# Optimization experiments

Hardware: AMD Instinct MI355X
Metric: run time of the kernel (lower is better)

Reference implementation:

```python
import jax, jax.numpy as jnp
import numpy as np

NUM_CLASSES = 33  # labels 0..32; class 0 = background, 32 instances
EPS = 1e-06


def _lovasz_hinge_flat(logits, labels):
    # logits, labels: flat 1-D float arrays (labels in {0,1})
    signs = 2.0 * labels - 1.0
    errors = 1.0 - logits * signs
    order = jnp.argsort(-errors)            # descending sort
    errors_sorted = errors[order]
    gt_sorted = labels[order]
    gts = jnp.sum(gt_sorted)
    intersection = gts - jnp.cumsum(gt_sorted)
    union = gts + jnp.cumsum(1.0 - gt_sorted)
    jaccard = 1.0 - intersection / union
    grad = jnp.concatenate([jaccard[:1], jaccard[1:] - jaccard[:-1]])
    return jnp.dot(jax.nn.relu(errors_sorted), grad)


def _per_sample_loss(y_emb, y_sig, gt_patch):
    # y_emb: [2,H,W] float, y_sig: [1,H,W] float, gt_patch: [1,H,W] int
    # to_onehot(gt)[0, 1:] -> [N,H,W], N = NUM_CLASSES-1 instance channels
    gt_one_hot = jax.nn.one_hot(gt_patch[0], NUM_CLASSES, axis=0, dtype=y_emb.dtype)[1:]
    counts = jnp.sum(gt_one_hot, axis=(1, 2), keepdims=True)          # [N,1,1]
    # per-instance embedding centers: [2,N,1,1]
    centers = jnp.sum(gt_one_hot[None] * y_emb[:, None], axis=(2, 3), keepdims=True) / counts
    instance_sigmas = gt_one_hot[None] * y_sig[:, None]               # [1,N,H,W]
    sigmas = jnp.sum(instance_sigmas, axis=(2, 3), keepdims=True) / counts  # [1,N,1,1]
    var_sigmas = jnp.sum(((instance_sigmas - jax.lax.stop_gradient(sigmas)) * gt_one_hot) ** 2) / counts  # [N,1,1]
    center_dist = jnp.linalg.norm(centers - y_emb[:, None], axis=0)   # [N,H,W]
    probs = jnp.exp(-0.5 * (center_dist / sigmas) ** 2)               # [1,N,H,W]
    logits = (probs * 2.0 - 1.0).reshape(-1)
    labels = jnp.broadcast_to(gt_one_hot[None], probs.shape).reshape(-1)
    return _lovasz_hinge_flat(logits, labels) + jnp.mean(var_sigmas)


def setup_inputs() -> dict:
    key = jax.random.key(0)
    k1, k2, k3 = jax.random.split(key, 3)
    B, H, W = 4, 512, 512
    y_embeddings = jax.random.normal(k1, (B, 2, H, W), dtype=jnp.float32)
    y_sigma = jax.random.uniform(k2, (B, 1, H, W), dtype=jnp.float32)
    y_true = jax.random.randint(k3, (B, 1, H, W), 0, NUM_CLASSES, dtype=jnp.int64)
    return {"y_embeddings": y_embeddings, "y_sigma": y_sigma, "y_true": y_true}


def reference(y_embeddings, y_sigma, y_true):
    # Assumes every sample contains foreground (random labels over 512x512
    # guarantee this w.h.p.), so the torch `if torch.any(gt>0)` branch is taken
    # for all samples and the final loss is the mean over the batch.
    losses = jax.vmap(_per_sample_loss)(y_embeddings, y_sigma, y_true)
    return jnp.mean(losses)
```

## Files before the change

### kernel.cpp

```cpp
#include <hip/hip_runtime.h>

#define HW    262144
#define BNUM  4
#define NC    33
#define NI    32

#define NB     2048
#define BSCALE 128.0f
#define EG     4096
#define ESCALE 2048.0f

typedef unsigned long long ull;

#define W_PART 16384
#define W_FIN  (W_PART + 5 * 33 * 256)

__global__ void __launch_bounds__(256) stats_kernel(
    const float* __restrict__ emb, const float* __restrict__ sig,
    const int* __restrict__ gt, float* __restrict__ ws) {
  int s = blockIdx.y;
  int j = blockIdx.x;
  int t = threadIdx.x;
  int w = t >> 6;
  __shared__ float acc[4][165];
  int bid = s * 64 + j;
  unsigned* wsu = (unsigned*)ws;
  if (t < 64) wsu[bid * 64 + t] = 0u;
  if (bid == 0 && t < 16) wsu[W_FIN + t] = 0u;
  for (int k = t; k < 4 * 165; k += 256) ((float*)acc)[k] = 0.f;
  __syncthreads();
  const float* e0p = emb + (size_t)s * 2 * HW;
  const float* e1p = e0p + HW;
  const float* sp  = sig + (size_t)s * HW;
  const int*   gp  = gt  + (size_t)s * HW;
  #pragma unroll
  for (int i = 0; i < 4; ++i) {
    int idx = j * 4096 + i * 1024 + t * 4;
    int4   lb = *(const int4*)(gp + idx);
    float4 x  = *(const float4*)(e0p + idx);
    float4 y  = *(const float4*)(e1p + idx);
    float4 sg = *(const float4*)(sp + idx);
#define ACC(L, X, Y, SG)                                                   \
    if (L > 0) {                                                           \
      atomicAdd(&acc[w][L], X);        atomicAdd(&acc[w][33 + L], Y);      \
      atomicAdd(&acc[w][66 + L], SG);  atomicAdd(&acc[w][99 + L], (SG)*(SG)); \
      atomicAdd(&acc[w][132 + L], 1.0f);                                   \
    }
    ACC(lb.x, x.x, y.x, sg.x)
    ACC(lb.y, x.y, y.y, sg.y)
    ACC(lb.z, x.z, y.z, sg.z)
    ACC(lb.w, x.w, y.w, sg.w)
#undef ACC
  }
  __syncthreads();
  if (t < 165) {
    float v = acc[0][t] + acc[1][t] + acc[2][t] + acc[3][t];
    ws[W_PART + t * 256 + s * 64 + j] = v;
  }
}

__global__ void __launch_bounds__(512) hist_scan_kernel(
    const float* __restrict__ emb, const int* __restrict__ gt,
    float* __restrict__ ws, float* __restrict__ out) {
  int s  = blockIdx.y;
  int lb = blockIdx.x;
  __shared__ unsigned hist[NB * 4];
  __shared__ float sums[165];
  __shared__ float4 cons[NC];
  __shared__ ull wsum[8];
  __shared__ float red[8];
  __shared__ float vart_s;
  __shared__ int flag;
  int t = threadIdx.x;
  int lane = t & 63, wid = t >> 6;
  for (int k = t; k < NB * 4; k += 512) hist[k] = 0u;
  if (t < 165) {
    const float4* pp = (const float4*)(ws + W_PART + t * 256 + s * 64);
    float sum = 0.f;
    #pragma unroll
    for (int i = 0; i < 16; ++i) { float4 v = pp[i]; sum += v.x + v.y + v.z + v.w; }
    sums[t] = sum;
  }
  __syncthreads();
  if (t >= 1 && t < NC) {
    float c = sums[132 + t];
    float4 C;
    if (c > 0.f) {
      float inv = 1.0f / c;
      float c0 = sums[t] * inv, c1 = sums[33 + t] * inv, sgm = sums[66 + t] * inv;
      float Q = 0.5f / (sgm * sgm) * BSCALE;
      C.x = Q; C.y = -2.0f * Q * c0; C.z = -2.0f * Q * c1;
      C.w = Q * (c0 * c0 + c1 * c1);
    } else {
      C.x = 0.f; C.y = 0.f; C.z = 0.f; C.w = (float)NB;
    }
    cons[t] = C;
  }
  __syncthreads();
  const float* e0p = emb + (size_t)s * 2 * HW;
  const float* e1p = e0p + HW;
  const int*   gp  = gt  + (size_t)s * HW;
  int idx = lb * 2048 + t * 4;
  int4   lbl = *(const int4*)(gp + idx);
  float4 px  = *(const float4*)(e0p + idx);
  float4 py  = *(const float4*)(e1p + idx);
  float4 ss;
  ss.x = fmaf(px.x, px.x, py.x * py.x);
  ss.y = fmaf(px.y, px.y, py.y * py.y);
  ss.z = fmaf(px.z, px.z, py.z * py.z);
  ss.w = fmaf(px.w, px.w, py.w * py.w);
  unsigned* hr = hist + (t & 3);
  #pragma unroll 4
  for (int n = 1; n <= NI; ++n) {
    float4 C = cons[n];
#define ITEM(P0, P1, SV, L)                                            \
    {                                                                  \
      float bf = fmaf(C.x, SV, fmaf(C.y, P0, fmaf(C.z, P1, C.w)));     \
      int ib = (int)bf;                                                \
      bool pos = (L == n);                                             \
      if (pos) ib = min(ib, NB - 1);                                   \
      if (ib < NB) atomicAdd(&hr[ib << 2], pos ? 0x10000u : 1u);       \
    }
    ITEM(px.x, py.x, ss.x, lbl.x)
    ITEM(px.y, py.y, ss.y, lbl.y)
    ITEM(px.z, py.z, ss.z, lbl.z)
    ITEM(px.w, py.w, ss.w, lbl.w)
#undef ITEM
  }
  __syncthreads();
  ull* th = ((ull*)ws) + (size_t)s * NB;
  for (int k = t; k < NB; k += 512) {
    unsigned v = hist[k*4] + hist[k*4+1] + hist[k*4+2] + hist[k*4+3];
    if (v) {
      ull add = ((ull)(v >> 16) << 32) | (v & 0xFFFFu);
      atomicAdd(&th[k], add);
    }
  }
  __syncthreads();
  if (t == 0) {
    __threadfence();
    unsigned* cnt = (unsigned*)(ws + W_FIN);
    flag = (atomicAdd(&cnt[8 + s], 1u) == 127u);
  }
  __syncthreads();
  if (!flag) return;

  unsigned* ep = hist;
  unsigned* en = hist + EG;
  for (int k = t; k < 2 * EG; k += 512) hist[k] = 0u;
  if (wid == 0) {
    float S = 0.f, rcp = 0.f;
    if (lane >= 1 && lane < NC) {
      float c = sums[132 + lane];
      if (c > 0.f) {
        float sg = sums[66 + lane] / c;
        S = sums[99 + lane] - c * sg * sg;
        rcp = 1.0f / c;
      }
    }
    for (int o = 32; o; o >>= 1) {
      S   += __shfl_down(S, o);
      rcp += __shfl_down(rcp, o);
    }
    if (lane == 0) vart_s = S * rcp / (float)NI;
  }
  __syncthreads();
  for (int b = t; b < NB; b += 512) {
    ull v = atomicAdd(&th[b], 0ull);
    unsigned pos = (unsigned)(v >> 32), neg = (unsigned)(v & 0xFFFFFFFFu);
    if (pos | neg) {
      float tc = ((float)b + 0.5f) * (1.0f / BSCALE);
      float ex = __expf(-tc);
      if (pos) {
        float e = 2.0f - 2.0f * ex;
        int k = (int)(e * ESCALE); if (k > EG - 1) k = EG - 1;
        atomicAdd(&ep[k], pos);
      }
      if (neg) {
        float e = 2.0f * ex;
        int k = (int)(e * ESCALE); if (k > EG - 1) k = EG - 1;
        atomicAdd(&en[k], neg);
      }
    }
  }
  __syncthreads();
  const int CH = EG / 512;
  int j0 = t * CH;
  unsigned np = 0, nn = 0;
  for (int k = 0; k < CH; ++k) {
    int b = EG - 1 - (j0 + k);
    np += ep[b]; nn += en[b];
  }
  ull v = ((ull)np << 32) | (ull)nn;
  ull inc = v;
  for (int o = 1; o < 64; o <<= 1) {
    ull u = __shfl_up(inc, o);
    if (lane >= o) inc += u;
  }
  if (lane == 63) wsum[wid] = inc;
  __syncthreads();
  ull offset = 0, total = 0;
  for (int i = 0; i < 8; ++i) {
    ull xr = wsum[i];
    if (i < wid) offset += xr;
    total += xr;
  }
  ull excl = offset + inc - v;
  float P = (float)(unsigned)(total >> 32);
  unsigned p = (unsigned)(excl >> 32), f = (unsigned)(excl & 0xFFFFFFFFu);
  float jprev = 1.0f - (P - (float)p) / (P + (float)f);
  float contrib = 0.f;
  for (int k = 0; k < CH; ++k) {
    int b = EG - 1 - (j0 + k);
    unsigned ap_ = ep[b], an_ = en[b];
    if (ap_ | an_) {
      p += ap_; f += an_;
      float j = 1.0f - (P - (float)p) / (P + (float)f);
      float e = ((float)b + 0.5f) * (2.0f / EG);
      contrib += e * (j - jprev);
      jprev = j;
    }
  }
  for (int o = 32; o; o >>= 1) contrib += __shfl_down(contrib, o);
  if (lane == 0) red[wid] = contrib;
  __syncthreads();
  if (t == 0) {
    float tot = 0.f;
    for (int i = 0; i < 8; ++i) tot += red[i];
    float loss = tot + vart_s;
    float* fin = ws + W_FIN;
    unsigned* cnt = (unsigned*)(fin + 4);
    atomicExch(&fin[s], loss);
    unsigned old = atomicAdd(&cnt[0], 1u);
    if (old == BNUM - 1) {
      float a = 0.f;
      for (int i = 0; i < BNUM; ++i) a += atomicAdd(&fin[i], 0.0f);
      out[0] = a * (1.0f / BNUM);
    }
  }
}

extern "C" void kernel_launch(void* const* d_in, const int* in_sizes, int n_in,
                              void* d_out, int out_size, void* d_ws, size_t ws_size,
                              hipStream_t stream) {
  const float* emb = (const float*)d_in[0];
  const float* sig = (const float*)d_in[1];
  const int*   gt  = (const int*)d_in[2];
  float* out = (float*)d_out;
  float* ws  = (float*)d_ws;

  dim3 gA(64, BNUM);
  stats_kernel<<<gA, 256, 0, stream>>>(emb, sig, gt, ws);
  dim3 gB(128, BNUM);
  hist_scan_kernel<<<gB, 512, 0, stream>>>(emb, gt, ws, out);
}
```

Measured before the change: 120.6 us.

## Fuse stats and histogram kernels with a per-sample grid barrier

Merges the stats kernel and the histogram/scan kernel into one launch of 512 blocks. Each block reads its pixels once, keeps them in registers, and writes partial stats. A spin-wait barrier across the 128 blocks of each sample then lets those partials be summed before binning. Workspace zeroing moves to a hipMemsetAsync, and shared memory for accumulators and histograms is overlaid in a union. This removes the second global read of embeddings and labels, but it depends on all 512 blocks being co-resident to avoid deadlock and adds spin-wait and memset overhead.

```diff
diff --git a/kernel.cpp b/kernel.cpp
--- a/kernel.cpp
+++ b/kernel.cpp
@@ -12,73 +12,85 @@
 
 typedef unsigned long long ull;
 
-#define W_PART 16384
-#define W_FIN  (W_PART + 5 * 33 * 256)
-
-__global__ void __launch_bounds__(256) stats_kernel(
+#define W_CNTA 16384
+#define W_CNTB 16388
+#define W_CNTF 16392
+#define W_FINL 16396
+#define MEMSET_BYTES (16400 * 4)
+#define W_PART 16400
+#define PJ 168
+#define PS (128 * PJ)
+
+union SMem {
+  float acc[8][165];
+  unsigned hist[NB * 4];
+};
+
+__global__ void __launch_bounds__(512, 4) fused_kernel(
     const float* __restrict__ emb, const float* __restrict__ sig,
-    const int* __restrict__ gt, float* __restrict__ ws) {
-  int s = blockIdx.y;
-  int j = blockIdx.x;
-  int t = threadIdx.x;
-  int w = t >> 6;
-  __shared__ float acc[4][165];
-  int bid = s * 64 + j;
-  unsigned* wsu = (unsigned*)ws;
-  if (t < 64) wsu[bid * 64 + t] = 0u;
-  if (bid == 0 && t < 16) wsu[W_FIN + t] = 0u;
-  for (int k = t; k < 4 * 165; k += 256) ((float*)acc)[k] = 0.f;
-  __syncthreads();
-  const float* e0p = emb + (size_t)s * 2 * HW;
-  const float* e1p = e0p + HW;
-  const float* sp  = sig + (size_t)s * HW;
-  const int*   gp  = gt  + (size_t)s * HW;
-  #pragma unroll
-  for (int i = 0; i < 4; ++i) {
-    int idx = j * 4096 + i * 1024 + t * 4;
-    int4   lb = *(const int4*)(gp + idx);
-    float4 x  = *(const float4*)(e0p + idx);
-    float4 y  = *(const float4*)(e1p + idx);
-    float4 sg = *(const float4*)(sp + idx);
-#define ACC(L, X, Y, SG)                                                   \
-    if (L > 0) {                                                           \
-      atomicAdd(&acc[w][L], X);        atomicAdd(&acc[w][33 + L], Y);      \
-      atomicAdd(&acc[w][66 + L], SG);  atomicAdd(&acc[w][99 + L], (SG)*(SG)); \
-      atomicAdd(&acc[w][132 + L], 1.0f);                                   \
-    }
-    ACC(lb.x, x.x, y.x, sg.x)
-    ACC(lb.y, x.y, y.y, sg.y)
-    ACC(lb.z, x.z, y.z, sg.z)
-    ACC(lb.w, x.w, y.w, sg.w)
-#undef ACC
-  }
-  __syncthreads();
-  if (t < 165) {
-    float v = acc[0][t] + acc[1][t] + acc[2][t] + acc[3][t];
-    ws[W_PART + t * 256 + s * 64 + j] = v;
-  }
-}
-
-__global__ void __launch_bounds__(512) hist_scan_kernel(
-    const float* __restrict__ emb, const int* __restrict__ gt,
-    float* __restrict__ ws, float* __restrict__ out) {
-  int s  = blockIdx.y;
-  int lb = blockIdx.x;
-  __shared__ unsigned hist[NB * 4];
+    const int* __restrict__ gt, float* __restrict__ ws,
+    float* __restrict__ out) {
+  __shared__ SMem sm;
   __shared__ float sums[165];
   __shared__ float4 cons[NC];
   __shared__ ull wsum[8];
   __shared__ float red[8];
   __shared__ float vart_s;
   __shared__ int flag;
+
   int t = threadIdx.x;
-  int lane = t & 63, wid = t >> 6;
-  for (int k = t; k < NB * 4; k += 512) hist[k] = 0u;
+  int bid = blockIdx.x;
+  int s = bid >> 7;
+  int lb = bid & 127;
+  int w = t >> 6;
+  int lane = t & 63, wid = w;
+
+  for (int k = t; k < 8 * 165; k += 512) ((float*)sm.acc)[k] = 0.f;
+  __syncthreads();
+  const float* e0p = emb + (size_t)s * 2 * HW;
+  const float* e1p = e0p + HW;
+  const float* sp  = sig + (size_t)s * HW;
+  const int*   gp  = gt  + (size_t)s * HW;
+  int idx = lb * 2048 + t * 4;
+  int4   lbl = *(const int4*)(gp + idx);
+  float4 x   = *(const float4*)(e0p + idx);
+  float4 y   = *(const float4*)(e1p + idx);
+  float4 sg4 = *(const float4*)(sp + idx);
+#define ACC(L, X, Y, SG)                                                     \
+  if (L > 0) {                                                               \
+    atomicAdd(&sm.acc[w][L], X);        atomicAdd(&sm.acc[w][33 + L], Y);    \
+    atomicAdd(&sm.acc[w][66 + L], SG);  atomicAdd(&sm.acc[w][99 + L], (SG)*(SG)); \
+    atomicAdd(&sm.acc[w][132 + L], 1.0f);                                    \
+  }
+  ACC(lbl.x, x.x, y.x, sg4.x)
+  ACC(lbl.y, x.y, y.y, sg4.y)
+  ACC(lbl.z, x.z, y.z, sg4.z)
+  ACC(lbl.w, x.w, y.w, sg4.w)
+#undef ACC
+  __syncthreads();
   if (t < 165) {
-    const float4* pp = (const float4*)(ws + W_PART + t * 256 + s * 64);
+    float v = 0.f;
+    #pragma unroll
+    for (int i = 0; i < 8; ++i) v += sm.acc[i][t];
+    ws[W_PART + s * PS + lb * PJ + t] = v;
+  }
+  {
+    unsigned* cntA = (unsigned*)ws + W_CNTA + s;
+    if (t == 0) {
+      __threadfence();
+      atomicAdd(cntA, 1u);
+      while (atomicAdd(cntA, 0u) < 128u) __builtin_amdgcn_s_sleep(2);
+      __threadfence();
+    }
+    __syncthreads();
+  }
+
+  for (int k = t; k < NB * 4; k += 512) sm.hist[k] = 0u;
+  if (t < 165) {
+    const float* pp = ws + W_PART + s * PS + t;
     float sum = 0.f;
-    #pragma unroll
-    for (int i = 0; i < 16; ++i) { float4 v = pp[i]; sum += v.x + v.y + v.z + v.w; }
+    #pragma unroll 8
+    for (int j = 0; j < 128; ++j) sum += pp[j * PJ];
     sums[t] = sum;
   }
   __syncthreads();
@@ -97,19 +109,12 @@
     cons[t] = C;
   }
   __syncthreads();
-  const float* e0p = emb + (size_t)s * 2 * HW;
-  const float* e1p = e0p + HW;
-  const int*   gp  = gt  + (size_t)s * HW;
-  int idx = lb * 2048 + t * 4;
-  int4   lbl = *(const int4*)(gp + idx);
-  float4 px  = *(const float4*)(e0p + idx);
-  float4 py  = *(const float4*)(e1p + idx);
   float4 ss;
-  ss.x = fmaf(px.x, px.x, py.x * py.x);
-  ss.y = fmaf(px.y, px.y, py.y * py.y);
-  ss.z = fmaf(px.z, px.z, py.z * py.z);
-  ss.w = fmaf(px.w, px.w, py.w * py.w);
-  unsigned* hr = hist + (t & 3);
+  ss.x = fmaf(x.x, x.x, y.x * y.x);
+  ss.y = fmaf(x.y, x.y, y.y * y.y);
+  ss.z = fmaf(x.z, x.z, y.z * y.z);
+  ss.w = fmaf(x.w, x.w, y.w * y.w);
+  unsigned* hr = sm.hist + (t & 3);
   #pragma unroll 4
   for (int n = 1; n <= NI; ++n) {
     float4 C = cons[n];
@@ -121,16 +126,16 @@
       if (pos) ib = min(ib, NB - 1);                                   \
       if (ib < NB) atomicAdd(&hr[ib << 2], pos ? 0x10000u : 1u);       \
     }
-    ITEM(px.x, py.x, ss.x, lbl.x)
-    ITEM(px.y, py.y, ss.y, lbl.y)
-    ITEM(px.z, py.z, ss.z, lbl.z)
-    ITEM(px.w, py.w, ss.w, lbl.w)
+    ITEM(x.x, y.x, ss.x, lbl.x)
+    ITEM(x.y, y.y, ss.y, lbl.y)
+    ITEM(x.z, y.z, ss.z, lbl.z)
+    ITEM(x.w, y.w, ss.w, lbl.w)
 #undef ITEM
   }
   __syncthreads();
   ull* th = ((ull*)ws) + (size_t)s * NB;
   for (int k = t; k < NB; k += 512) {
-    unsigned v = hist[k*4] + hist[k*4+1] + hist[k*4+2] + hist[k*4+3];
+    unsigned v = sm.hist[k*4] + sm.hist[k*4+1] + sm.hist[k*4+2] + sm.hist[k*4+3];
     if (v) {
       ull add = ((ull)(v >> 16) << 32) | (v & 0xFFFFu);
       atomicAdd(&th[k], add);
@@ -139,22 +144,21 @@
   __syncthreads();
   if (t == 0) {
     __threadfence();
-    unsigned* cnt = (unsigned*)(ws + W_FIN);
-    flag = (atomicAdd(&cnt[8 + s], 1u) == 127u);
+    flag = (atomicAdd((unsigned*)ws + W_CNTB + s, 1u) == 127u);
   }
   __syncthreads();
   if (!flag) return;
 
-  unsigned* ep = hist;
-  unsigned* en = hist + EG;
-  for (int k = t; k < 2 * EG; k += 512) hist[k] = 0u;
+  unsigned* ep = sm.hist;
+  unsigned* en = sm.hist + EG;
+  for (int k = t; k < 2 * EG; k += 512) sm.hist[k] = 0u;
   if (wid == 0) {
     float S = 0.f, rcp = 0.f;
     if (lane >= 1 && lane < NC) {
       float c = sums[132 + lane];
       if (c > 0.f) {
-        float sg = sums[66 + lane] / c;
-        S = sums[99 + lane] - c * sg * sg;
+        float sgm = sums[66 + lane] / c;
+        S = sums[99 + lane] - c * sgm * sgm;
         rcp = 1.0f / c;
       }
     }
@@ -228,11 +232,12 @@
     float tot = 0.f;
     for (int i = 0; i < 8; ++i) tot += red[i];
     float loss = tot + vart_s;
-    float* fin = ws + W_FIN;
-    unsigned* cnt = (unsigned*)(fin + 4);
+    float* fin = ws + W_FINL;
     atomicExch(&fin[s], loss);
-    unsigned old = atomicAdd(&cnt[0], 1u);
+    __threadfence();
+    unsigned old = atomicAdd((unsigned*)ws + W_CNTF, 1u);
     if (old == BNUM - 1) {
+      __threadfence();
       float a = 0.f;
       for (int i = 0; i < BNUM; ++i) a += atomicAdd(&fin[i], 0.0f);
       out[0] = a * (1.0f / BNUM);
@@ -249,8 +254,6 @@
   float* out = (float*)d_out;
   float* ws  = (float*)d_ws;
 
-  dim3 gA(64, BNUM);
-  stats_kernel<<<gA, 256, 0, stream>>>(emb, sig, gt, ws);
-  dim3 gB(128, BNUM);
-  hist_scan_kernel<<<gB, 512, 0, stream>>>(emb, gt, ws, out);
+  hipMemsetAsync(d_ws, 0, MEMSET_BYTES, stream);
+  fused_kernel<<<512, 512, 0, stream>>>(emb, sig, gt, ws, out);
 }
```

Measured after the change: 145.6 us. +20.8%, slower.

## Halve histogram bins, double stats blocks, and reorganize partial-sum workspace layout

Applied to the files above, without the earlier changes.

Halves the coarse threshold histogram from 2048 to 1024 bins at half the scale, which cuts shared-memory zeroing, the global merge atomics and the finalize pass. The stats kernel now runs twice as many blocks, each over half the pixels, to raise parallelism. Per-block partials are stored contiguously per block and summed with strided loads, and the counters move to a compact fixed region. The coarser bins lower the accuracy of the Lovasz approximation, and the stats reduction now reads 128 partials per value instead of 64.

```diff
diff --git a/kernel.cpp b/kernel.cpp
--- a/kernel.cpp
+++ b/kernel.cpp
@@ -5,15 +5,19 @@
 #define NC    33
 #define NI    32
 
-#define NB     2048
-#define BSCALE 128.0f
+#define NB     1024
+#define BSCALE 64.0f
 #define EG     4096
 #define ESCALE 2048.0f
 
 typedef unsigned long long ull;
 
-#define W_PART 16384
-#define W_FIN  (W_PART + 5 * 33 * 256)
+#define W_CNTB 8192
+#define W_CNTF 8196
+#define W_FINL 8200
+#define W_PART 8208
+#define PJ 168
+#define PS (128 * PJ)
 
 __global__ void __launch_bounds__(256) stats_kernel(
     const float* __restrict__ emb, const float* __restrict__ sig,
@@ -23,10 +27,12 @@
   int t = threadIdx.x;
   int w = t >> 6;
   __shared__ float acc[4][165];
-  int bid = s * 64 + j;
+  int bid = s * 128 + j;
   unsigned* wsu = (unsigned*)ws;
-  if (t < 64) wsu[bid * 64 + t] = 0u;
-  if (bid == 0 && t < 16) wsu[W_FIN + t] = 0u;
+  if (t < 16) {
+    wsu[bid * 16 + t] = 0u;
+    if (bid == 0) wsu[8192 + t] = 0u;
+  }
   for (int k = t; k < 4 * 165; k += 256) ((float*)acc)[k] = 0.f;
   __syncthreads();
   const float* e0p = emb + (size_t)s * 2 * HW;
@@ -34,8 +40,8 @@
   const float* sp  = sig + (size_t)s * HW;
   const int*   gp  = gt  + (size_t)s * HW;
   #pragma unroll
-  for (int i = 0; i < 4; ++i) {
-    int idx = j * 4096 + i * 1024 + t * 4;
+  for (int i = 0; i < 2; ++i) {
+    int idx = j * 2048 + i * 1024 + t * 4;
     int4   lb = *(const int4*)(gp + idx);
     float4 x  = *(const float4*)(e0p + idx);
     float4 y  = *(const float4*)(e1p + idx);
@@ -55,7 +61,7 @@
   __syncthreads();
   if (t < 165) {
     float v = acc[0][t] + acc[1][t] + acc[2][t] + acc[3][t];
-    ws[W_PART + t * 256 + s * 64 + j] = v;
+    ws[W_PART + s * PS + j * PJ + t] = v;
   }
 }
 
@@ -64,7 +70,7 @@
     float* __restrict__ ws, float* __restrict__ out) {
   int s  = blockIdx.y;
   int lb = blockIdx.x;
-  __shared__ unsigned hist[NB * 4];
+  __shared__ unsigned hist[EG * 2];
   __shared__ float sums[165];
   __shared__ float4 cons[NC];
   __shared__ ull wsum[8];
@@ -75,10 +81,10 @@
   int lane = t & 63, wid = t >> 6;
   for (int k = t; k < NB * 4; k += 512) hist[k] = 0u;
   if (t < 165) {
-    const float4* pp = (const float4*)(ws + W_PART + t * 256 + s * 64);
+    const float* pp = ws + W_PART + s * PS + t;
     float sum = 0.f;
-    #pragma unroll
-    for (int i = 0; i < 16; ++i) { float4 v = pp[i]; sum += v.x + v.y + v.z + v.w; }
+    #pragma unroll 8
+    for (int j = 0; j < 128; ++j) sum += pp[j * PJ];
     sums[t] = sum;
   }
   __syncthreads();
@@ -139,8 +145,7 @@
   __syncthreads();
   if (t == 0) {
     __threadfence();
-    unsigned* cnt = (unsigned*)(ws + W_FIN);
-    flag = (atomicAdd(&cnt[8 + s], 1u) == 127u);
+    flag = (atomicAdd((unsigned*)ws + W_CNTB + s, 1u) == 127u);
   }
   __syncthreads();
   if (!flag) return;
@@ -228,10 +233,10 @@
     float tot = 0.f;
     for (int i = 0; i < 8; ++i) tot += red[i];
     float loss = tot + vart_s;
-    float* fin = ws + W_FIN;
-    unsigned* cnt = (unsigned*)(fin + 4);
+    float* fin = ws + W_FINL;
     atomicExch(&fin[s], loss);
-    unsigned old = atomicAdd(&cnt[0], 1u);
+    __threadfence();
+    unsigned old = atomicAdd((unsigned*)ws + W_CNTF, 1u);
     if (old == BNUM - 1) {
       float a = 0.f;
       for (int i = 0; i < BNUM; ++i) a += atomicAdd(&fin[i], 0.0f);
@@ -249,7 +254,7 @@
   float* out = (float*)d_out;
   float* ws  = (float*)d_ws;
 
-  dim3 gA(64, BNUM);
+  dim3 gA(128, BNUM);
   stats_kernel<<<gA, 256, 0, stream>>>(emb, sig, gt, ws);
   dim3 gB(128, BNUM);
   hist_scan_kernel<<<gB, 512, 0, stream>>>(emb, gt, ws, out);
```

Result: faster. 118.0 us (median of 2 runs) (-2.2%).
